# Optimization experiments

Hardware: AMD Instinct MI355X
Metric: run time of the kernel (lower is better)

Reference implementation:

```python
import jax, jax.numpy as jnp
import numpy as np

N_NODES = 50000
N_EDGES = 800000   # avg degree ~16
IN_CH = 128
HID = 64


def setup_inputs() -> dict:
    key = jax.random.key(0)
    k0, k1, k2, k3 = jax.random.split(key, 4)
    x = jax.random.normal(k0, (N_NODES, IN_CH), dtype=jnp.float32)
    edge_index = jax.random.randint(k1, (2, N_EDGES), 0, N_NODES, dtype=jnp.int32)
    # Glorot-ish init like torch GCNConv
    W1 = jax.random.normal(k2, (IN_CH, HID), dtype=jnp.float32) / np.sqrt(IN_CH).astype(np.float32)
    b1 = jnp.zeros((HID,), dtype=jnp.float32)
    W2 = jax.random.normal(k3, (HID, HID), dtype=jnp.float32) / np.sqrt(HID).astype(np.float32)
    b2 = jnpp = jnp.zeros((HID,), dtype=jnp.float32)
    return {"x": x, "edge_index": edge_index, "W1": W1, "b1": b1, "W2": W2, "b2": b2}


def gcn_conv(x, src, dst, W, b, n):
    """GCNConv with self-loops already appended to (src, dst).
    out = D^{-1/2} (A + I) D^{-1/2} (x @ W) + b, symmetric normalization."""
    h = x @ W                                        # [N, out]
    deg = jax.ops.segment_sum(jnp.ones(src.shape, jnp.float32), dst, num_segments=n)
    dinv = jax.lax.rsqrt(jnp.maximum(deg, 1.0))      # deg >= 1 due to self-loops
    norm = dinv[src] * dinv[dst]                     # [E+N]
    msg = h[src] * norm[:, None]                     # gather + scale
    return jax.ops.segment_sum(msg, dst, num_segments=n) + b


def reference(x, edge_index, W1, b1, W2, b2):
    n = x.shape[0]
    loop = jnp.arange(n, dtype=edge_index.dtype)
    src = jnp.concatenate([edge_index[0], loop])     # add self-loops
    dst = jnp.concatenate([edge_index[1], loop])
    # encode: GCNConv -> ReLU -> GCNConv
    z = jax.nn.relu(gcn_conv(x, src, dst, W1, b1, n))
    z = gcn_conv(z, src, dst, W2, b2, n)
    # decode: gather endpoint embeddings, elementwise product, reduce over hidden
    return (z[edge_index[0]] * z[edge_index[1]]).sum(axis=1)   # [E]
```

## Files before the change

### kernel.cpp

```cpp
#include <hip/hip_runtime.h>
#include <hip/hip_fp16.h>

#define INCH 128
#define HIDC 64
#define CAP  64

typedef int            v4i __attribute__((ext_vector_type(4)));
typedef float          v4f __attribute__((ext_vector_type(4)));
typedef float          v2f __attribute__((ext_vector_type(2)));
typedef unsigned int   v4u __attribute__((ext_vector_type(4)));

__device__ inline float2 u2f(unsigned int u) {
    return __half22float2(__builtin_bit_cast(__half2, u));
}
__device__ inline unsigned int f2u(float a, float b) {
    __half2 h = __float22half2_rn(make_float2(a, b));
    return __builtin_bit_cast(unsigned int, h);
}

__global__ __launch_bounds__(128, 2) void build_gemm1_kernel(const int* __restrict__ src,
                                                             const int* __restrict__ dst,
                                                             int* __restrict__ count,
                                                             unsigned short* __restrict__ col,
                                                             const float* __restrict__ x,
                                                             const float* __restrict__ W,
                                                             __half* __restrict__ hs,
                                                             int E, int N, int EB) {
    int b = (int)blockIdx.x;
    if (b < EB) {
        int i8 = (b * 128 + (int)threadIdx.x) * 8;
        if (i8 + 7 < E) {
            v4i sa = __builtin_nontemporal_load((const v4i*)(src + i8));
            v4i sb = __builtin_nontemporal_load((const v4i*)(src + i8 + 4));
            v4i da = __builtin_nontemporal_load((const v4i*)(dst + i8));
            v4i db = __builtin_nontemporal_load((const v4i*)(dst + i8 + 4));
            int rs[8], ds[8], ss[8];
            ds[0]=da.x; ds[1]=da.y; ds[2]=da.z; ds[3]=da.w;
            ds[4]=db.x; ds[5]=db.y; ds[6]=db.z; ds[7]=db.w;
            ss[0]=sa.x; ss[1]=sa.y; ss[2]=sa.z; ss[3]=sa.w;
            ss[4]=sb.x; ss[5]=sb.y; ss[6]=sb.z; ss[7]=sb.w;
            #pragma unroll
            for (int k = 0; k < 8; ++k) rs[k] = atomicAdd(&count[ds[k]], 1);
            #pragma unroll
            for (int k = 0; k < 8; ++k)
                if (rs[k] < CAP) col[ds[k] * CAP + rs[k]] = (unsigned short)ss[k];
        } else {
            for (int i = i8; i < E; ++i) {
                int d = dst[i];
                int r = atomicAdd(&count[d], 1);
                if (r < CAP) col[d * CAP + r] = (unsigned short)src[i];
            }
        }
    } else {
        int nb = b - EB;
        int node = (nb >> 1) * 128 + (int)threadIdx.x;
        int ch0 = (nb & 1) * 32;
        if (node >= N) return;
        const float4* xr = (const float4*)(x + (size_t)node * INCH);
        float acc[32];
        #pragma unroll
        for (int c = 0; c < 32; ++c) acc[c] = 0.f;
        for (int kc = 0; kc < INCH / 4; ++kc) {
            float4 xk = xr[kc];
            const float* wr = W + (kc * 4) * HIDC + ch0;
            #pragma unroll
            for (int ch = 0; ch < 32; ++ch) acc[ch] = fmaf(xk.x, wr[ch], acc[ch]);
            #pragma unroll
            for (int ch = 0; ch < 32; ++ch) acc[ch] = fmaf(xk.y, wr[HIDC + ch], acc[ch]);
            #pragma unroll
            for (int ch = 0; ch < 32; ++ch) acc[ch] = fmaf(xk.z, wr[2 * HIDC + ch], acc[ch]);
            #pragma unroll
            for (int ch = 0; ch < 32; ++ch) acc[ch] = fmaf(xk.w, wr[3 * HIDC + ch], acc[ch]);
        }
        v4u hv[4];
        #pragma unroll
        for (int k = 0; k < 4; ++k) {
            #pragma unroll
            for (int e = 0; e < 4; ++e) {
                int c2 = k * 4 + e;
                hv[k][e] = f2u(acc[2 * c2], acc[2 * c2 + 1]);
            }
        }
        v4u* hr = (v4u*)(hs + (size_t)node * HIDC + ch0);
        #pragma unroll
        for (int k = 0; k < 4; ++k) hr[k] = hv[k];
    }
}

__global__ __launch_bounds__(256) void scale_kernel(const int* __restrict__ count,
                                                    __half* __restrict__ hs, int N) {
    int idx = (int)blockIdx.x * 256 + threadIdx.x;
    if (idx >= N * 8) return;
    int node = idx >> 3;
    float dn = rsqrtf((float)count[node] + 1.0f);
    v4u v = ((const v4u*)hs)[idx];
    v4u o;
    #pragma unroll
    for (int k = 0; k < 4; ++k) {
        float2 f = u2f(v[k]);
        o[k] = f2u(dn * f.x, dn * f.y);
    }
    ((v4u*)hs)[idx] = o;
}

__global__ __launch_bounds__(128, 2) void gemm2_kernel(const __half* __restrict__ agg1,
                                                       const float* __restrict__ W,
                                                       const int* __restrict__ count,
                                                       __half* __restrict__ hs, int N) {
    int node = (blockIdx.x >> 1) * 128 + threadIdx.x;
    int ch0 = (blockIdx.x & 1) * 32;
    if (node >= N) return;
    const v4u* ar = (const v4u*)(agg1 + (size_t)node * HIDC);
    float acc[32];
    #pragma unroll
    for (int c = 0; c < 32; ++c) acc[c] = 0.f;
    for (int kc = 0; kc < HIDC / 8; ++kc) {
        v4u av = ar[kc];
        #pragma unroll
        for (int k2 = 0; k2 < 4; ++k2) {
            float2 f = u2f(av[k2]);
            float v0 = fmaxf(f.x, 0.f);
            float v1 = fmaxf(f.y, 0.f);
            const float* wr = W + (kc * 8 + k2 * 2) * HIDC + ch0;
            #pragma unroll
            for (int ch = 0; ch < 32; ++ch) acc[ch] = fmaf(v0, wr[ch], acc[ch]);
            #pragma unroll
            for (int ch = 0; ch < 32; ++ch) acc[ch] = fmaf(v1, wr[HIDC + ch], acc[ch]);
        }
    }
    float dn = rsqrtf((float)count[node] + 1.0f);
    v4u hv[4];
    #pragma unroll
    for (int k = 0; k < 4; ++k) {
        #pragma unroll
        for (int e = 0; e < 4; ++e) {
            int c2 = k * 4 + e;
            hv[k][e] = f2u(dn * acc[2 * c2], dn * acc[2 * c2 + 1]);
        }
    }
    v4u* hr = (v4u*)(hs + (size_t)node * HIDC + ch0);
    #pragma unroll
    for (int k = 0; k < 4; ++k) hr[k] = hv[k];
}

__global__ __launch_bounds__(256) void aggregate_kernel(const int* __restrict__ count,
                                                        const unsigned short* __restrict__ col,
                                                        const __half* __restrict__ hs,
                                                        const float* __restrict__ bias,
                                                        __half* __restrict__ agg, int N) {
    int node = blockIdx.x * 8 + (threadIdx.x >> 5);
    int c2 = threadIdx.x & 31;
    if (node >= N) return;
    int cnt = count[node];
    int deg = cnt < CAP ? cnt : CAP;
    const unsigned int* h2p = (const unsigned int*)hs;
    float2 acc = u2f(h2p[(size_t)node * 32 + c2]);
    const unsigned short* row = col + (size_t)node * CAP;
    for (int jb = 0; jb < deg; jb += 16) {
        int s[16];
        unsigned int v[16];
        #pragma unroll
        for (int u = 0; u < 16; ++u) {
            int idx = jb + u;
            s[u] = row[idx < deg ? idx : jb];
        }
        #pragma unroll
        for (int u = 0; u < 16; ++u)
            v[u] = h2p[(size_t)s[u] * 32 + c2];
        #pragma unroll
        for (int u = 0; u < 16; ++u) {
            if (jb + u < deg) {
                float2 f = u2f(v[u]);
                acc.x += f.x; acc.y += f.y;
            }
        }
    }
    float dn = rsqrtf((float)cnt + 1.0f);
    float2 bb = *(const float2*)(bias + c2 * 2);
    ((unsigned int*)agg)[(size_t)node * 32 + c2] =
        f2u(fmaf(acc.x, dn, bb.x), fmaf(acc.y, dn, bb.y));
}

__global__ __launch_bounds__(256) void decode_kernel(const int* __restrict__ src,
                                                     const int* __restrict__ dst,
                                                     const __half* __restrict__ z,
                                                     float* __restrict__ out, int E) {
    long long tid = (long long)blockIdx.x * 256 + threadIdx.x;
    int g = (int)(tid >> 3);
    int q = threadIdx.x & 7;
    int e0 = g * 4;
    if (e0 >= E) return;
    const v4u* z8 = (const v4u*)z;
    bool full = (e0 + 3 < E);
    int s[4], d[4];
    if (full) {
        v4i sv = __builtin_nontemporal_load((const v4i*)(src + e0));
        v4i dv = __builtin_nontemporal_load((const v4i*)(dst + e0));
        s[0]=sv.x; s[1]=sv.y; s[2]=sv.z; s[3]=sv.w;
        d[0]=dv.x; d[1]=dv.y; d[2]=dv.z; d[3]=dv.w;
    } else {
        #pragma unroll
        for (int k = 0; k < 4; ++k) {
            int e = e0 + k < E ? e0 + k : e0;
            s[k] = src[e]; d[k] = dst[e];
        }
    }
    v4u a[4], b[4];
    #pragma unroll
    for (int k = 0; k < 4; ++k) a[k] = z8[(size_t)s[k] * 8 + q];
    #pragma unroll
    for (int k = 0; k < 4; ++k) b[k] = z8[(size_t)d[k] * 8 + q];
    float p[4];
    #pragma unroll
    for (int k = 0; k < 4; ++k) {
        float acc = 0.f;
        #pragma unroll
        for (int j = 0; j < 4; ++j) {
            float2 fa = u2f(a[k][j]);
            float2 fb = u2f(b[k][j]);
            acc = fmaf(fa.x, fb.x, acc);
            acc = fmaf(fa.y, fb.y, acc);
        }
        p[k] = acc;
    }
    #pragma unroll
    for (int m = 4; m; m >>= 1) {
        #pragma unroll
        for (int k = 0; k < 4; ++k) p[k] += __shfl_xor(p[k], m, 64);
    }
    if (q == 0) {
        if (full) {
            v4f r; r.x = p[0]; r.y = p[1]; r.z = p[2]; r.w = p[3];
            __builtin_nontemporal_store(r, (v4f*)(out + e0));
        } else {
            for (int k = 0; k < 4 && e0 + k < E; ++k) out[e0 + k] = p[k];
        }
    }
}

extern "C" void kernel_launch(void* const* d_in, const int* in_sizes, int n_in,
                              void* d_out, int out_size, void* d_ws, size_t ws_size,
                              hipStream_t stream) {
    const float* x  = (const float*)d_in[0];
    const int*   ei = (const int*)d_in[1];
    const float* W1 = (const float*)d_in[2];
    const float* b1 = (const float*)d_in[3];
    const float* W2 = (const float*)d_in[4];
    const float* b2 = (const float*)d_in[5];
    float* out = (float*)d_out;

    const int hid  = in_sizes[3];
    const int inch = in_sizes[2] / hid;
    const int N    = in_sizes[0] / inch;
    const int E    = in_sizes[1] / 2;
    const int* srcp = ei;
    const int* dstp = ei + E;

    char* p = (char*)d_ws;
    auto alloc = [&](size_t bytes) { char* r = p; p += (bytes + 255) & ~(size_t)255; return r; };
    int*            count = (int*)alloc((size_t)N * 4);
    unsigned short* col   = (unsigned short*)alloc((size_t)N * CAP * 2);
    __half*         h1s   = (__half*)alloc((size_t)N * HIDC * 2);
    __half*         h2s   = (__half*)alloc((size_t)N * HIDC * 2);
    __half*         zt    = (__half*)alloc((size_t)N * HIDC * 2);
    __half*         agg1  = (__half*)alloc((size_t)N * HIDC * 2);

    (void)hipMemsetAsync(count, 0, (size_t)N * 4, stream);

    int EB = (E / 8 + 127) / 128 + 1;
    int GB = 2 * ((N + 127) / 128);
    build_gemm1_kernel<<<EB + GB, 128, 0, stream>>>(srcp, dstp, count, col,
                                                    x, W1, h1s, E, N, EB);
    scale_kernel<<<(N * 8 + 255) / 256, 256, 0, stream>>>(count, h1s, N);

    aggregate_kernel<<<(N + 7) / 8, 256, 0, stream>>>(count, col, h1s, b1, agg1, N);
    gemm2_kernel<<<GB, 128, 0, stream>>>(agg1, W2, count, h2s, N);
    aggregate_kernel<<<(N + 7) / 8, 256, 0, stream>>>(count, col, h2s, b2, zt, N);

    long long groups = ((long long)E + 3) / 4;
    long long blocksD = (groups * 8 + 255) / 256;
    decode_kernel<<<(int)blocksD, 256, 0, stream>>>(srcp, dstp, zt, out, E);
}
```

Measured before the change: 213.3 us.

## Fuse first-layer aggregation with second GEMM via wave shuffles

Merges the layer-1 neighbor aggregation and the W2 GEMM into one kernel. Each 32-lane group aggregates a node, applies bias and ReLU, then computes the 64x64 projection with wave shuffles against W2 staged in shared memory, so the agg1 intermediate is never written or re-read. It also remaps the GEMM1 blocks so each 128-thread block covers 64 nodes with both channel halves together, which should improve x row reuse. The tradeoff is that every aggregation block now loads W2 into LDS and runs a serial shuffle loop, which adds per-node compute.

```diff
diff --git a/kernel.cpp b/kernel.cpp
--- a/kernel.cpp
+++ b/kernel.cpp
@@ -7,7 +7,6 @@
 
 typedef int            v4i __attribute__((ext_vector_type(4)));
 typedef float          v4f __attribute__((ext_vector_type(4)));
-typedef float          v2f __attribute__((ext_vector_type(2)));
 typedef unsigned int   v4u __attribute__((ext_vector_type(4)));
 
 __device__ inline float2 u2f(unsigned int u) {
@@ -53,8 +52,9 @@
         }
     } else {
         int nb = b - EB;
-        int node = (nb >> 1) * 128 + (int)threadIdx.x;
-        int ch0 = (nb & 1) * 32;
+        int lane = (int)threadIdx.x & 63;
+        int ch0 = ((int)threadIdx.x >> 6) * 32;
+        int node = nb * 64 + lane;
         if (node >= N) return;
         const float4* xr = (const float4*)(x + (size_t)node * INCH);
         float acc[32];
@@ -103,44 +103,63 @@
     ((v4u*)hs)[idx] = o;
 }
 
-__global__ __launch_bounds__(128, 2) void gemm2_kernel(const __half* __restrict__ agg1,
-                                                       const float* __restrict__ W,
-                                                       const int* __restrict__ count,
-                                                       __half* __restrict__ hs, int N) {
-    int node = (blockIdx.x >> 1) * 128 + threadIdx.x;
-    int ch0 = (blockIdx.x & 1) * 32;
+__global__ __launch_bounds__(256) void agg1_gemm2_kernel(const int* __restrict__ count,
+                                                         const unsigned short* __restrict__ col,
+                                                         const __half* __restrict__ hs1,
+                                                         const float* __restrict__ b1,
+                                                         const float* __restrict__ W2,
+                                                         __half* __restrict__ h2s, int N) {
+    __shared__ float2 W2L[HIDC * 32];
+    for (int i = threadIdx.x; i < HIDC * 32; i += 256)
+        W2L[i] = ((const float2*)W2)[i];
+    __syncthreads();
+
+    int node = blockIdx.x * 8 + (threadIdx.x >> 5);
+    int l = threadIdx.x & 31;
+    int lane = threadIdx.x & 63;
+    int gbase = lane & 32;
     if (node >= N) return;
-    const v4u* ar = (const v4u*)(agg1 + (size_t)node * HIDC);
-    float acc[32];
-    #pragma unroll
-    for (int c = 0; c < 32; ++c) acc[c] = 0.f;
-    for (int kc = 0; kc < HIDC / 8; ++kc) {
-        v4u av = ar[kc];
-        #pragma unroll
-        for (int k2 = 0; k2 < 4; ++k2) {
-            float2 f = u2f(av[k2]);
-            float v0 = fmaxf(f.x, 0.f);
-            float v1 = fmaxf(f.y, 0.f);
-            const float* wr = W + (kc * 8 + k2 * 2) * HIDC + ch0;
-            #pragma unroll
-            for (int ch = 0; ch < 32; ++ch) acc[ch] = fmaf(v0, wr[ch], acc[ch]);
-            #pragma unroll
-            for (int ch = 0; ch < 32; ++ch) acc[ch] = fmaf(v1, wr[HIDC + ch], acc[ch]);
-        }
-    }
-    float dn = rsqrtf((float)count[node] + 1.0f);
-    v4u hv[4];
-    #pragma unroll
-    for (int k = 0; k < 4; ++k) {
-        #pragma unroll
-        for (int e = 0; e < 4; ++e) {
-            int c2 = k * 4 + e;
-            hv[k][e] = f2u(dn * acc[2 * c2], dn * acc[2 * c2 + 1]);
-        }
-    }
-    v4u* hr = (v4u*)(hs + (size_t)node * HIDC + ch0);
-    #pragma unroll
-    for (int k = 0; k < 4; ++k) hr[k] = hv[k];
+    int cnt = count[node];
+    int deg = cnt < CAP ? cnt : CAP;
+    const unsigned int* h2p = (const unsigned int*)hs1;
+    float2 acc = u2f(h2p[(size_t)node * 32 + l]);
+    const unsigned short* row = col + (size_t)node * CAP;
+    for (int jb = 0; jb < deg; jb += 16) {
+        int s[16];
+        unsigned int v[16];
+        #pragma unroll
+        for (int u = 0; u < 16; ++u) {
+            int idx = jb + u;
+            s[u] = row[idx < deg ? idx : jb];
+        }
+        #pragma unroll
+        for (int u = 0; u < 16; ++u)
+            v[u] = h2p[(size_t)s[u] * 32 + l];
+        #pragma unroll
+        for (int u = 0; u < 16; ++u) {
+            if (jb + u < deg) {
+                float2 f = u2f(v[u]);
+                acc.x += f.x; acc.y += f.y;
+            }
+        }
+    }
+    float dn = rsqrtf((float)cnt + 1.0f);
+    float2 bb = *(const float2*)(b1 + l * 2);
+    float rx = fmaxf(fmaf(acc.x, dn, bb.x), 0.f);
+    float ry = fmaxf(fmaf(acc.y, dn, bb.y), 0.f);
+
+    float hx = 0.f, hy = 0.f;
+    #pragma unroll
+    for (int j = 0; j < 32; ++j) {
+        int srcLane = gbase + j;
+        float ax = __shfl(rx, srcLane, 64);
+        float ay = __shfl(ry, srcLane, 64);
+        float2 w0 = W2L[(2 * j) * 32 + l];
+        float2 w1 = W2L[(2 * j + 1) * 32 + l];
+        hx = fmaf(ax, w0.x, hx); hy = fmaf(ax, w0.y, hy);
+        hx = fmaf(ay, w1.x, hx); hy = fmaf(ay, w1.y, hy);
+    }
+    ((unsigned int*)h2s)[(size_t)node * 32 + l] = f2u(dn * hx, dn * hy);
 }
 
 __global__ __launch_bounds__(256) void aggregate_kernel(const int* __restrict__ count,
@@ -263,18 +282,16 @@
     __half*         h1s   = (__half*)alloc((size_t)N * HIDC * 2);
     __half*         h2s   = (__half*)alloc((size_t)N * HIDC * 2);
     __half*         zt    = (__half*)alloc((size_t)N * HIDC * 2);
-    __half*         agg1  = (__half*)alloc((size_t)N * HIDC * 2);
 
     (void)hipMemsetAsync(count, 0, (size_t)N * 4, stream);
 
     int EB = (E / 8 + 127) / 128 + 1;
-    int GB = 2 * ((N + 127) / 128);
+    int GB = (N + 63) / 64;
     build_gemm1_kernel<<<EB + GB, 128, 0, stream>>>(srcp, dstp, count, col,
                                                     x, W1, h1s, E, N, EB);
     scale_kernel<<<(N * 8 + 255) / 256, 256, 0, stream>>>(count, h1s, N);
 
-    aggregate_kernel<<<(N + 7) / 8, 256, 0, stream>>>(count, col, h1s, b1, agg1, N);
-    gemm2_kernel<<<GB, 128, 0, stream>>>(agg1, W2, count, h2s, N);
+    agg1_gemm2_kernel<<<(N + 7) / 8, 256, 0, stream>>>(count, col, h1s, b1, W2, h2s, N);
     aggregate_kernel<<<(N + 7) / 8, 256, 0, stream>>>(count, col, h2s, b2, zt, N);
 
     long long groups = ((long long)E + 3) / 4;
```

Measured after the change: 268.1 us. 1.26x slower.
